# Kernel optimization log

Measured on AMD Instinct MI355X. Metric: run time of the kernel, lower is better.

The kernel has to match this reference:

```python
import jax, jax.numpy as jnp
import numpy as np

B = 65536
NEGO = 48        # num_ego_obs
NADO = 24        # num_ado_obs
NTEAMS, TSIZE = 2, 3
NA = NTEAMS * TSIZE          # num_agents = 6
NADOAG = NA - 1              # 5 ado agents
E = 256                      # embed_dims[-1]
H = 4                        # attention heads
AD = 256 // H                # attend_dim = 64


def setup_inputs() -> dict:
    key = jax.random.key(0)
    ks = jax.random.split(key, 16)
    w = lambda k, shape: jax.random.normal(k, shape, jnp.float32) * 0.05
    return {
        "observations": jax.random.normal(ks[0], (B, NEGO + NADOAG * NADO), jnp.float32),
        # ego encoder: Linear(48,256)+LeakyReLU, Linear(256,256)+LeakyReLU
        "ego_w0": w(ks[1], (NEGO, E)), "ego_b0": jnp.zeros((E,), jnp.float32),
        "ego_w1": w(ks[2], (E, E)),    "ego_b1": jnp.zeros((E,), jnp.float32),
        # ado encoder: Linear(25,256)+LeakyReLU, Linear(256,256)+LeakyReLU
        "ado_w0": w(ks[3], (NADO + 1, E)), "ado_b0": jnp.zeros((E,), jnp.float32),
        "ado_w1": w(ks[4], (E, E)),        "ado_b1": jnp.zeros((E,), jnp.float32),
        # per-head extractors stacked on a leading head axis
        "key_w": w(ks[5], (H, E, AD)),   # no bias
        "sel_w": w(ks[6], (H, E, AD)),   # no bias
        "lat_w": w(ks[7], (H, E, AD)), "lat_b": jnp.zeros((H, AD), jnp.float32),
        # projection: Linear(256, 64)
        "proj_w": w(ks[8], (H * AD, AD)), "proj_b": jnp.zeros((AD,), jnp.float32),
    }


def reference(observations, ego_w0, ego_b0, ego_w1, ego_b1,
              ado_w0, ado_b0, ado_w1, ado_b1,
              key_w, sel_w, lat_w, lat_b, proj_w, proj_b):
    lrelu = jax.nn.leaky_relu  # slope 0.01, matches nn.LeakyReLU()
    obs_ego = observations[:, :NEGO]                              # [B, 48]
    obs_ado = observations[:, NEGO:NEGO + NADOAG * NADO]          # [B, 120]
    team_ids = jnp.asarray([t for t in range(NTEAMS) for _ in range(TSIZE)],
                           jnp.float32)                           # [6]

    # ego latent [B, E]
    ego = lrelu(lrelu(obs_ego @ ego_w0 + ego_b0) @ ego_w1 + ego_b1)

    # ado_ag_obs[..., ado_id::5] == reshape(B, NADO, 5)[:, :, ado_id]
    ado_obs = obs_ado.reshape(-1, NADO, NADOAG).transpose(0, 2, 1)  # [B, 5, 24]
    tid = jnp.broadcast_to(team_ids[1:NA][None, :, None],
                           (ado_obs.shape[0], NADOAG, 1))           # [B, 5, 1]
    ado_in = jnp.concatenate([ado_obs, tid], axis=-1)               # [B, 5, 25]
    ado = lrelu(lrelu(ado_in @ ado_w0 + ado_b0) @ ado_w1 + ado_b1)  # [B, 5, E]

    slct = jnp.einsum('be,hed->bhd', ego, sel_w)                    # [B, H, AD]
    keys = jnp.einsum('bne,hed->bnhd', ado, key_w)                  # [B, 5, H, AD]
    lats = lrelu(jnp.einsum('bne,hed->bnhd', ado, lat_w) + lat_b)   # [B, 5, H, AD]

    logits = jnp.einsum('bhd,bnhd->bhn', slct, keys) / jnp.sqrt(jnp.float32(AD))
    attn = jax.nn.softmax(logits, axis=-1)                          # [B, H, 5]
    agg = jnp.einsum('bhn,bnhd->bhd', attn, lats).reshape(-1, H * AD)  # heads concat in order
    proj = agg @ proj_w + proj_b                                    # [B, 64]
    return jnp.concatenate([obs_ego, proj], axis=-1)                # [B, 112]
```

## Files before the change

### kernel.cpp

```cpp
#include <hip/hip_runtime.h>
#include <hip/hip_bf16.h>


typedef __bf16 bf16x8 __attribute__((ext_vector_type(8)));
typedef __bf16 bf16x4 __attribute__((ext_vector_type(4)));
typedef float  f32x4  __attribute__((ext_vector_type(4)));

#define OFF_EGO0 0
#define OFF_EGO1 16384
#define OFF_ADO0 81920
#define OFF_ADO1 90112
#define OFF_SEL  155648
#define OFF_KEY  221184
#define OFF_LAT  286720
#define OFF_PROJ 352256
#define WS_ELEMS 368640

__global__ __launch_bounds__(256) void prep_weights(
    const float* __restrict__ ew0, const float* __restrict__ ew1,
    const float* __restrict__ aw0, const float* __restrict__ aw1,
    const float* __restrict__ keyw, const float* __restrict__ selw,
    const float* __restrict__ latw, const float* __restrict__ projw,
    __bf16* __restrict__ ws)
{
  int i = blockIdx.x * 256 + threadIdx.x;
  if (i >= WS_ELEMS) return;
  float v;
  if (i < OFF_EGO1)      { int j=i;          int c=j>>6, k=j&63;  v = (k<48) ? ew0[k*256+c] : 0.f; }
  else if (i < OFF_ADO0) { int j=i-OFF_EGO1; int c=j>>8, k=j&255; v = ew1[k*256+c]; }
  else if (i < OFF_ADO1) { int j=i-OFF_ADO0; int c=j>>5, k=j&31;  v = (k<25) ? aw0[k*256+c] : 0.f; }
  else if (i < OFF_SEL)  { int j=i-OFF_ADO1; int c=j>>8, k=j&255; v = aw1[k*256+c]; }
  else if (i < OFF_KEY)  { int j=i-OFF_SEL;  int c=j>>8, k=j&255; v = selw[(c>>6)*16384 + k*64 + (c&63)]; }
  else if (i < OFF_LAT)  { int j=i-OFF_KEY;  int c=j>>8, k=j&255; v = keyw[(c>>6)*16384 + k*64 + (c&63)]; }
  else if (i < OFF_PROJ) { int j=i-OFF_LAT;  int c=j>>8, k=j&255; v = latw[(c>>6)*16384 + k*64 + (c&63)]; }
  else                   { int j=i-OFF_PROJ; int c=j>>8, k=j&255; v = projw[k*64+c]; }
  ws[i] = (__bf16)v;
}

__device__ __forceinline__ bf16x8 lds_loadA(const __bf16* base, int row, int kByte, int rowBytes) {
  int off = (row * rowBytes + kByte) ^ ((row & 7) << 4);
  return *reinterpret_cast<const bf16x8*>(reinterpret_cast<const char*>(base) + off);
}
__device__ __forceinline__ void lds_store_bf16(__bf16* base, int row, int col, __bf16 v) {
  int off = (row * 512 + col * 2) ^ ((row & 7) << 4);
  *reinterpret_cast<__bf16*>(reinterpret_cast<char*>(base) + off) = v;
}

#define P_ADO2   0
#define P_EGOIN  0
#define P_EGOH1  2048
#define P_ADOIN  24576
#define P_EGOH2  40960
#define P_PROJIN 40960
#define P_H1     49152
#define P_OBSRAW 49152
#define P_OUT    73728
#define POOL_BYTES 77824

template<int KP, int R, int C, bool ACT>
__device__ __forceinline__ void gemm_block(const __bf16* __restrict__ sA, int aRow0,
                                           __bf16* __restrict__ sC, int cRow0,
                                           const __bf16* __restrict__ WT,
                                           const float* __restrict__ bias,
                                           int w, int lr, int lg)
{
  constexpr int NKB = KP / 32;
  static_assert(NKB % C == 0, "chunk must divide NKB");
  f32x4 acc[R][2];
  #pragma unroll
  for (int t = 0; t < R; ++t) {
    acc[t][0] = f32x4{0.f,0.f,0.f,0.f};
    acc[t][1] = f32x4{0.f,0.f,0.f,0.f};
  }
  const int col0 = w*32 + lr;
  #pragma unroll
  for (int kc = 0; kc < NKB; kc += C) {
    bf16x8 bfr[C][2];
    #pragma unroll
    for (int j = 0; j < C; ++j)
      #pragma unroll
      for (int c2 = 0; c2 < 2; ++c2)
        bfr[j][c2] = *reinterpret_cast<const bf16x8*>(
            WT + (col0 + c2*16)*KP + (kc+j)*32 + lg*8);
    bf16x8 af[C][R];
    #pragma unroll
    for (int j = 0; j < C; ++j)
      #pragma unroll
      for (int t = 0; t < R; ++t)
        af[j][t] = lds_loadA(sA, aRow0 + t*16 + lr, (kc+j)*64 + lg*16, KP*2);
    #pragma unroll
    for (int j = 0; j < C; ++j)
      #pragma unroll
      for (int c2 = 0; c2 < 2; ++c2)
        #pragma unroll
        for (int t = 0; t < R; ++t)
          acc[t][c2] = __builtin_amdgcn_mfma_f32_16x16x32_bf16(af[j][t], bfr[j][c2], acc[t][c2], 0, 0, 0);
  }
  #pragma unroll
  for (int c2 = 0; c2 < 2; ++c2) {
    const int col = col0 + c2*16;
    const float bv = bias[col];
    #pragma unroll
    for (int t = 0; t < R; ++t) {
      #pragma unroll
      for (int e = 0; e < 4; ++e) {
        float x = acc[t][c2][e] + bv;
        if (ACT) x = x > 0.f ? x : 0.01f * x;
        lds_store_bf16(sC, cRow0 + t*16 + lg*4 + e, col, (__bf16)x);
      }
    }
  }
}

__global__ __launch_bounds__(512, 2) void fused_kernel(
    const float* __restrict__ obs,
    const float* __restrict__ eb0, const float* __restrict__ eb1,
    const float* __restrict__ ab0, const float* __restrict__ ab1,
    const float* __restrict__ latb, const float* __restrict__ projb,
    const __bf16* __restrict__ ws,
    float* __restrict__ out)
{
  const int tid = threadIdx.x;
  const int w  = tid >> 6;
  const int l  = tid & 63;
  const int lr = l & 15;
  const int lg = l >> 4;
  const int b0 = blockIdx.x * 16;

  __shared__ __align__(16) char pool[POOL_BYTES];
  __bf16* sEgoIn = reinterpret_cast<__bf16*>(pool + P_EGOIN);
  __bf16* sEgoH1 = reinterpret_cast<__bf16*>(pool + P_EGOH1);
  __bf16* sAdoIn = reinterpret_cast<__bf16*>(pool + P_ADOIN);
  __bf16* sEgoH2 = reinterpret_cast<__bf16*>(pool + P_EGOH2);
  __bf16* sProj  = reinterpret_cast<__bf16*>(pool + P_PROJIN);
  __bf16* sAdo2  = reinterpret_cast<__bf16*>(pool + P_ADO2);
  __bf16* sH1    = reinterpret_cast<__bf16*>(pool + P_H1);
  float*  sObsF  = reinterpret_cast<float*>(pool + P_OBSRAW);
  float*  sLogF  = reinterpret_cast<float*>(pool + P_OUT);
  float*  sOutF  = reinterpret_cast<float*>(pool + P_OUT);

  {
    const f32x4* o4 = reinterpret_cast<const f32x4*>(obs);
    #pragma unroll
    for (int idx = tid; idx < 672; idx += 512) {
      int row = idx / 42, c4 = idx % 42;
      f32x4 v = __builtin_nontemporal_load(o4 + (size_t)(b0+row)*42 + c4);
      *reinterpret_cast<f32x4*>(sObsF + row*168 + c4*4) = v;
      if (c4 < 12)
        __builtin_nontemporal_store(v,
            reinterpret_cast<f32x4*>(out + (size_t)(b0+row)*112 + c4*4));
    }
  }
  __syncthreads();

  {
    if (tid < 192) {
      int row = tid / 12, c4 = tid % 12;
      f32x4 v = *reinterpret_cast<const f32x4*>(sObsF + row*168 + c4*4);
      bf16x4 bv = { (__bf16)v[0], (__bf16)v[1], (__bf16)v[2], (__bf16)v[3] };
      int off = (row*128 + c4*8) ^ ((row&7)<<4);
      *reinterpret_cast<bf16x4*>(reinterpret_cast<char*>(sEgoIn) + off) = bv;
    } else if (tid < 256) {
      int t = tid - 192;
      int row = t >> 2, ch = t & 3;
      bf16x4 z = {};
      int off = (row*128 + 96 + ch*8) ^ ((row&7)<<4);
      *reinterpret_cast<bf16x4*>(reinterpret_cast<char*>(sEgoIn) + off) = z;
    }
    if (tid >= 256 && tid < 496) {
      int t = tid - 256;
      int ldsrow = t / 3, p = t % 3;
      int n = ldsrow >> 4, r = ldsrow & 15;
      const float* orow = sObsF + r*168 + 48;
      bf16x8 v;
      #pragma unroll
      for (int j = 0; j < 8; ++j) v[j] = (__bf16)orow[(p*8+j)*5 + n];
      int off = (ldsrow*64 + p*16) ^ ((ldsrow&7)<<4);
      *reinterpret_cast<bf16x8*>(reinterpret_cast<char*>(sAdoIn) + off) = v;
    }
    if (tid >= 432) {
      int t = tid - 432;
      int n = t >> 4;
      bf16x8 v = {};
      v[0] = (__bf16)((n >= 2) ? 1.0f : 0.0f);
      int off = (t*64 + 48) ^ ((t&7)<<4);
      *reinterpret_cast<bf16x8*>(reinterpret_cast<char*>(sAdoIn) + off) = v;
    }
  }
  __syncthreads();

  gemm_block<64, 1, 2, true>(sEgoIn, 0, sEgoH1, 0, ws + OFF_EGO0, eb0, w, lr, lg);
  gemm_block<32, 3, 1, true>(sAdoIn, 0, sH1,    0, ws + OFF_ADO0, ab0, w, lr, lg);
  __syncthreads();

  gemm_block<256, 1, 8, true>(sEgoH1, 0, sEgoH2, 0, ws + OFF_EGO1, eb1, w, lr, lg);
  __syncthreads();

  f32x4 slct[2];
  {
    const __bf16* WT = ws + OFF_SEL;
    slct[0] = f32x4{0.f,0.f,0.f,0.f};
    slct[1] = f32x4{0.f,0.f,0.f,0.f};
    #pragma unroll
    for (int kc = 0; kc < 8; kc += 4) {
      bf16x8 bfr[4][2];
      #pragma unroll
      for (int j = 0; j < 4; ++j)
        #pragma unroll
        for (int c2 = 0; c2 < 2; ++c2)
          bfr[j][c2] = *reinterpret_cast<const bf16x8*>(
              WT + (w*32 + c2*16 + lr)*256 + (kc+j)*32 + lg*8);
      bf16x8 af[4];
      #pragma unroll
      for (int j = 0; j < 4; ++j)
        af[j] = lds_loadA(sEgoH2, lr, (kc+j)*64 + lg*16, 512);
      #pragma unroll
      for (int j = 0; j < 4; ++j)
        #pragma unroll
        for (int c2 = 0; c2 < 2; ++c2)
          slct[c2] = __builtin_amdgcn_mfma_f32_16x16x32_bf16(af[j], bfr[j][c2], slct[c2], 0, 0, 0);
    }
    slct[0] *= 0.125f;
    slct[1] *= 0.125f;
  }
  gemm_block<256, 3, 4, true>(sH1, 0, sAdo2, 0, ws + OFF_ADO1, ab1, w, lr, lg);
  __syncthreads();

  gemm_block<32, 2, 1, true>(sAdoIn, 48, sH1, 0, ws + OFF_ADO0, ab0, w, lr, lg);
  __syncthreads();

  gemm_block<256, 2, 4, true>(sH1, 0, sAdo2, 48, ws + OFF_ADO1, ab1, w, lr, lg);
  __syncthreads();

  f32x4 part[5];
  {
    const __bf16* WK = ws + OFF_KEY;
    f32x4 kacc[5][2];
    #pragma unroll
    for (int n = 0; n < 5; ++n) {
      kacc[n][0] = f32x4{0.f,0.f,0.f,0.f};
      kacc[n][1] = f32x4{0.f,0.f,0.f,0.f};
    }
    #pragma unroll
    for (int kc = 0; kc < 8; kc += 2) {
      bf16x8 bk[2][2];
      #pragma unroll
      for (int j = 0; j < 2; ++j)
        #pragma unroll
        for (int c2 = 0; c2 < 2; ++c2)
          bk[j][c2] = *reinterpret_cast<const bf16x8*>(
              WK + (w*32 + c2*16 + lr)*256 + (kc+j)*32 + lg*8);
      bf16x8 af[2][5];
      #pragma unroll
      for (int j = 0; j < 2; ++j)
        #pragma unroll
        for (int n = 0; n < 5; ++n)
          af[j][n] = lds_loadA(sAdo2, n*16 + lr, (kc+j)*64 + lg*16, 512);
      #pragma unroll
      for (int j = 0; j < 2; ++j)
        #pragma unroll
        for (int c2 = 0; c2 < 2; ++c2)
          #pragma unroll
          for (int n = 0; n < 5; ++n)
            kacc[n][c2] = __builtin_amdgcn_mfma_f32_16x16x32_bf16(af[j][n], bk[j][c2], kacc[n][c2], 0, 0, 0);
    }
    #pragma unroll
    for (int n = 0; n < 5; ++n)
      part[n] = kacc[n][0]*slct[0] + kacc[n][1]*slct[1];
  }
  #pragma unroll
  for (int n = 0; n < 5; ++n) {
    #pragma unroll
    for (int m = 1; m < 16; m <<= 1) {
      part[n][0] += __shfl_xor(part[n][0], m);
      part[n][1] += __shfl_xor(part[n][1], m);
      part[n][2] += __shfl_xor(part[n][2], m);
      part[n][3] += __shfl_xor(part[n][3], m);
    }
  }
  #pragma unroll
  for (int n = 0; n < 5; ++n)
    if (lr == n)
      *reinterpret_cast<f32x4*>(sLogF + (w*5 + n)*16 + lg*4) = part[n];
  __syncthreads();
  {
    #pragma unroll
    for (int n = 0; n < 5; ++n)
      part[n] = *reinterpret_cast<const f32x4*>(sLogF + (w*5 + n)*16 + lg*4)
              + *reinterpret_cast<const f32x4*>(sLogF + ((w^1)*5 + n)*16 + lg*4);
    f32x4 mx = part[0];
    #pragma unroll
    for (int n = 1; n < 5; ++n)
      #pragma unroll
      for (int e = 0; e < 4; ++e) mx[e] = fmaxf(mx[e], part[n][e]);
    f32x4 s = f32x4{0.f,0.f,0.f,0.f};
    #pragma unroll
    for (int n = 0; n < 5; ++n) {
      #pragma unroll
      for (int e = 0; e < 4; ++e) part[n][e] = __expf(part[n][e] - mx[e]);
      s += part[n];
    }
    f32x4 inv;
    #pragma unroll
    for (int e = 0; e < 4; ++e) inv[e] = 1.0f / s[e];
    #pragma unroll
    for (int n = 0; n < 5; ++n) part[n] *= inv;
  }

  f32x4 agg[2];
  agg[0] = f32x4{0.f,0.f,0.f,0.f};
  agg[1] = f32x4{0.f,0.f,0.f,0.f};
  {
    const __bf16* WL = ws + OFF_LAT;
    f32x4 lacc[5][2];
    #pragma unroll
    for (int n = 0; n < 5; ++n) {
      lacc[n][0] = f32x4{0.f,0.f,0.f,0.f};
      lacc[n][1] = f32x4{0.f,0.f,0.f,0.f};
    }
    #pragma unroll
    for (int kc = 0; kc < 8; kc += 2) {
      bf16x8 bl[2][2];
      #pragma unroll
      for (int j = 0; j < 2; ++j)
        #pragma unroll
        for (int c2 = 0; c2 < 2; ++c2)
          bl[j][c2] = *reinterpret_cast<const bf16x8*>(
              WL + (w*32 + c2*16 + lr)*256 + (kc+j)*32 + lg*8);
      bf16x8 af[2][5];
      #pragma unroll
      for (int j = 0; j < 2; ++j)
        #pragma unroll
        for (int n = 0; n < 5; ++n)
          af[j][n] = lds_loadA(sAdo2, n*16 + lr, (kc+j)*64 + lg*16, 512);
      #pragma unroll
      for (int j = 0; j < 2; ++j)
        #pragma unroll
        for (int c2 = 0; c2 < 2; ++c2)
          #pragma unroll
          for (int n = 0; n < 5; ++n)
            lacc[n][c2] = __builtin_amdgcn_mfma_f32_16x16x32_bf16(af[j][n], bl[j][c2], lacc[n][c2], 0, 0, 0);
    }
    #pragma unroll
    for (int c2 = 0; c2 < 2; ++c2) {
      const float lb = latb[w*32 + c2*16 + lr];
      #pragma unroll
      for (int n = 0; n < 5; ++n) {
        #pragma unroll
        for (int e = 0; e < 4; ++e) {
          float x = lacc[n][c2][e] + lb;
          x = x > 0.f ? x : 0.01f * x;
          agg[c2][e] += part[n][e] * x;
        }
      }
    }
  }
  #pragma unroll
  for (int c2 = 0; c2 < 2; ++c2)
    #pragma unroll
    for (int e = 0; e < 4; ++e)
      lds_store_bf16(sProj, lg*4 + e, w*32 + c2*16 + lr, (__bf16)agg[c2][e]);
  __syncthreads();

  if (w < 4) {
    const __bf16* WT = ws + OFF_PROJ;
    f32x4 pacc = f32x4{0.f,0.f,0.f,0.f};
    #pragma unroll
    for (int kc = 0; kc < 8; kc += 4) {
      bf16x8 bfr[4];
      #pragma unroll
      for (int j = 0; j < 4; ++j)
        bfr[j] = *reinterpret_cast<const bf16x8*>(WT + (w*16+lr)*256 + (kc+j)*32 + lg*8);
      bf16x8 af[4];
      #pragma unroll
      for (int j = 0; j < 4; ++j)
        af[j] = lds_loadA(sProj, lr, (kc+j)*64 + lg*16, 512);
      #pragma unroll
      for (int j = 0; j < 4; ++j)
        pacc = __builtin_amdgcn_mfma_f32_16x16x32_bf16(af[j], bfr[j], pacc, 0, 0, 0);
    }
    const float pb = projb[w*16 + lr];
    #pragma unroll
    for (int e = 0; e < 4; ++e)
      sOutF[(lg*4 + e)*64 + w*16 + lr] = pacc[e] + pb;
  }
  __syncthreads();

  if (tid < 256) {
    int row = tid >> 4, q = tid & 15;
    f32x4 v = *reinterpret_cast<const f32x4*>(sOutF + row*64 + q*4);
    __builtin_nontemporal_store(v,
        reinterpret_cast<f32x4*>(out + (size_t)(b0+row)*112 + 48 + q*4));
  }
}

extern "C" void kernel_launch(void* const* d_in, const int* in_sizes, int n_in,
                              void* d_out, int out_size, void* d_ws, size_t ws_size,
                              hipStream_t stream) {
  const float* obs   = (const float*)d_in[0];
  const float* ew0   = (const float*)d_in[1];
  const float* eb0   = (const float*)d_in[2];
  const float* ew1   = (const float*)d_in[3];
  const float* eb1   = (const float*)d_in[4];
  const float* aw0   = (const float*)d_in[5];
  const float* ab0   = (const float*)d_in[6];
  const float* aw1   = (const float*)d_in[7];
  const float* ab1   = (const float*)d_in[8];
  const float* keyw  = (const float*)d_in[9];
  const float* selw  = (const float*)d_in[10];
  const float* latw  = (const float*)d_in[11];
  const float* latb  = (const float*)d_in[12];
  const float* projw = (const float*)d_in[13];
  const float* projb = (const float*)d_in[14];
  __bf16* ws = (__bf16*)d_ws;
  float* out = (float*)d_out;

  prep_weights<<<dim3((WS_ELEMS + 255)/256), dim3(256), 0, stream>>>(
      ew0, ew1, aw0, aw1, keyw, selw, latw, projw, ws);
  fused_kernel<<<dim3(65536/16), dim3(512), 0, stream>>>(
      obs, eb0, eb1, ab0, ab1, latb, projb, ws, out);
}
```

Before: 498.4 us.

## Cut register pressure to run four blocks per CU

Raises the launch-bounds minimum from two to four blocks per multiprocessor, which tightens the per-thread register budget. To fit that budget, several GEMM calls use a smaller k-unroll template parameter. The key and latent projections now loop over the two column halves one at a time instead of keeping both accumulators live. The A fragments are reloaded from LDS for each half, which adds LDS traffic and cuts instruction-level parallelism in exchange for more waves in flight. LDS per block may still cap occupancy, and the compiler may spill registers.

```diff
diff --git a/kernel.cpp b/kernel.cpp
--- a/kernel.cpp
+++ b/kernel.cpp
@@ -112,7 +112,7 @@
   }
 }
 
-__global__ __launch_bounds__(512, 2) void fused_kernel(
+__global__ __launch_bounds__(512, 4) void fused_kernel(
     const float* __restrict__ obs,
     const float* __restrict__ eb0, const float* __restrict__ eb1,
     const float* __restrict__ ab0, const float* __restrict__ ab1,
@@ -193,7 +193,7 @@
   gemm_block<32, 3, 1, true>(sAdoIn, 0, sH1,    0, ws + OFF_ADO0, ab0, w, lr, lg);
   __syncthreads();
 
-  gemm_block<256, 1, 8, true>(sEgoH1, 0, sEgoH2, 0, ws + OFF_EGO1, eb1, w, lr, lg);
+  gemm_block<256, 1, 4, true>(sEgoH1, 0, sEgoH2, 0, ws + OFF_EGO1, eb1, w, lr, lg);
   __syncthreads();
 
   f32x4 slct[2];
@@ -223,50 +223,47 @@
     slct[0] *= 0.125f;
     slct[1] *= 0.125f;
   }
-  gemm_block<256, 3, 4, true>(sH1, 0, sAdo2, 0, ws + OFF_ADO1, ab1, w, lr, lg);
+  gemm_block<256, 3, 2, true>(sH1, 0, sAdo2, 0, ws + OFF_ADO1, ab1, w, lr, lg);
   __syncthreads();
 
   gemm_block<32, 2, 1, true>(sAdoIn, 48, sH1, 0, ws + OFF_ADO0, ab0, w, lr, lg);
   __syncthreads();
 
-  gemm_block<256, 2, 4, true>(sH1, 0, sAdo2, 48, ws + OFF_ADO1, ab1, w, lr, lg);
+  gemm_block<256, 2, 2, true>(sH1, 0, sAdo2, 48, ws + OFF_ADO1, ab1, w, lr, lg);
   __syncthreads();
 
   f32x4 part[5];
+  #pragma unroll
+  for (int n = 0; n < 5; ++n) part[n] = f32x4{0.f,0.f,0.f,0.f};
   {
     const __bf16* WK = ws + OFF_KEY;
-    f32x4 kacc[5][2];
-    #pragma unroll
-    for (int n = 0; n < 5; ++n) {
-      kacc[n][0] = f32x4{0.f,0.f,0.f,0.f};
-      kacc[n][1] = f32x4{0.f,0.f,0.f,0.f};
-    }
-    #pragma unroll
-    for (int kc = 0; kc < 8; kc += 2) {
-      bf16x8 bk[2][2];
-      #pragma unroll
-      for (int j = 0; j < 2; ++j)
-        #pragma unroll
-        for (int c2 = 0; c2 < 2; ++c2)
-          bk[j][c2] = *reinterpret_cast<const bf16x8*>(
-              WK + (w*32 + c2*16 + lr)*256 + (kc+j)*32 + lg*8);
-      bf16x8 af[2][5];
-      #pragma unroll
-      for (int j = 0; j < 2; ++j)
-        #pragma unroll
-        for (int n = 0; n < 5; ++n)
-          af[j][n] = lds_loadA(sAdo2, n*16 + lr, (kc+j)*64 + lg*16, 512);
-      #pragma unroll
-      for (int j = 0; j < 2; ++j)
-        #pragma unroll
-        for (int c2 = 0; c2 < 2; ++c2)
+    #pragma unroll
+    for (int c2 = 0; c2 < 2; ++c2) {
+      const int col = w*32 + c2*16 + lr;
+      f32x4 kacc[5];
+      #pragma unroll
+      for (int n = 0; n < 5; ++n) kacc[n] = f32x4{0.f,0.f,0.f,0.f};
+      #pragma unroll
+      for (int kc = 0; kc < 8; kc += 2) {
+        bf16x8 bk[2];
+        #pragma unroll
+        for (int j = 0; j < 2; ++j)
+          bk[j] = *reinterpret_cast<const bf16x8*>(WK + col*256 + (kc+j)*32 + lg*8);
+        bf16x8 af[2][5];
+        #pragma unroll
+        for (int j = 0; j < 2; ++j)
           #pragma unroll
           for (int n = 0; n < 5; ++n)
-            kacc[n][c2] = __builtin_amdgcn_mfma_f32_16x16x32_bf16(af[j][n], bk[j][c2], kacc[n][c2], 0, 0, 0);
-    }
-    #pragma unroll
-    for (int n = 0; n < 5; ++n)
-      part[n] = kacc[n][0]*slct[0] + kacc[n][1]*slct[1];
+            af[j][n] = lds_loadA(sAdo2, n*16 + lr, (kc+j)*64 + lg*16, 512);
+        #pragma unroll
+        for (int j = 0; j < 2; ++j)
+          #pragma unroll
+          for (int n = 0; n < 5; ++n)
+            kacc[n] = __builtin_amdgcn_mfma_f32_16x16x32_bf16(af[j][n], bk[j], kacc[n], 0, 0, 0);
+      }
+      #pragma unroll
+      for (int n = 0; n < 5; ++n) part[n] += kacc[n] * slct[c2];
+    }
   }
   #pragma unroll
   for (int n = 0; n < 5; ++n) {
@@ -312,43 +309,36 @@
   agg[1] = f32x4{0.f,0.f,0.f,0.f};
   {
     const __bf16* WL = ws + OFF_LAT;
-    f32x4 lacc[5][2];
-    #pragma unroll
-    for (int n = 0; n < 5; ++n) {
-      lacc[n][0] = f32x4{0.f,0.f,0.f,0.f};
-      lacc[n][1] = f32x4{0.f,0.f,0.f,0.f};
-    }
-    #pragma unroll
-    for (int kc = 0; kc < 8; kc += 2) {
-      bf16x8 bl[2][2];
-      #pragma unroll
-      for (int j = 0; j < 2; ++j)
-        #pragma unroll
-        for (int c2 = 0; c2 < 2; ++c2)
-          bl[j][c2] = *reinterpret_cast<const bf16x8*>(
-              WL + (w*32 + c2*16 + lr)*256 + (kc+j)*32 + lg*8);
-      bf16x8 af[2][5];
-      #pragma unroll
-      for (int j = 0; j < 2; ++j)
-        #pragma unroll
-        for (int n = 0; n < 5; ++n)
-          af[j][n] = lds_loadA(sAdo2, n*16 + lr, (kc+j)*64 + lg*16, 512);
-      #pragma unroll
-      for (int j = 0; j < 2; ++j)
-        #pragma unroll
-        for (int c2 = 0; c2 < 2; ++c2)
+    #pragma unroll
+    for (int c2 = 0; c2 < 2; ++c2) {
+      const int col = w*32 + c2*16 + lr;
+      f32x4 lacc[5];
+      #pragma unroll
+      for (int n = 0; n < 5; ++n) lacc[n] = f32x4{0.f,0.f,0.f,0.f};
+      #pragma unroll
+      for (int kc = 0; kc < 8; kc += 2) {
+        bf16x8 bl[2];
+        #pragma unroll
+        for (int j = 0; j < 2; ++j)
+          bl[j] = *reinterpret_cast<const bf16x8*>(WL + col*256 + (kc+j)*32 + lg*8);
+        bf16x8 af[2][5];
+        #pragma unroll
+        for (int j = 0; j < 2; ++j)
           #pragma unroll
           for (int n = 0; n < 5; ++n)
-            lacc[n][c2] = __builtin_amdgcn_mfma_f32_16x16x32_bf16(af[j][n], bl[j][c2], lacc[n][c2], 0, 0, 0);
-    }
-    #pragma unroll
-    for (int c2 = 0; c2 < 2; ++c2) {
-      const float lb = latb[w*32 + c2*16 + lr];
+            af[j][n] = lds_loadA(sAdo2, n*16 + lr, (kc+j)*64 + lg*16, 512);
+        #pragma unroll
+        for (int j = 0; j < 2; ++j)
+          #pragma unroll
+          for (int n = 0; n < 5; ++n)
+            lacc[n] = __builtin_amdgcn_mfma_f32_16x16x32_bf16(af[j][n], bl[j], lacc[n], 0, 0, 0);
+      }
+      const float lb = latb[col];
       #pragma unroll
       for (int n = 0; n < 5; ++n) {
         #pragma unroll
         for (int e = 0; e < 4; ++e) {
-          float x = lacc[n][c2][e] + lb;
+          float x = lacc[n][e] + lb;
           x = x > 0.f ? x : 0.01f * x;
           agg[c2][e] += part[n][e] * x;
         }
```

Measured after the change: 470.9 us. 1.06x faster.
